# Kernel tuning notes

Hardware: AMD Instinct MI355X
Metric: run time of the kernel (lower is better)

## Reference

```python
import jax, jax.numpy as jnp
import numpy as np

N = 100000      # nodes
E = 1600000     # nnz of precomputed A^K (avg degree 16)
D = 64          # in_feats
C = 64          # n_classes
LN_EPS = 1e-5


def setup_inputs() -> dict:
    key = jax.random.key(0)
    ks = jax.random.split(key, 8)
    feat = jax.random.normal(ks[0], (N, D), dtype=jnp.float32)
    feat_ori = jax.random.normal(ks[1], (N, D), dtype=jnp.float32)
    row = jax.random.randint(ks[2], (E,), 0, N)
    col = jax.random.randint(ks[3], (E,), 0, N)
    adj_vals = jax.random.uniform(ks[4], (E,), dtype=jnp.float32)
    # Linear params (xavier_uniform weight, zero bias)
    limit = float(np.sqrt(6.0 / (D + C)))
    W = jax.random.uniform(ks[5], (C, D), dtype=jnp.float32, minval=-limit, maxval=limit)
    b = jnp.zeros((C,), dtype=jnp.float32)
    # LayerNorm params
    gamma = jnp.ones((C,), dtype=jnp.float32)
    beta = jnp.zeros((C,), dtype=jnp.float32)
    return {"feat": feat, "feat_ori": feat_ori, "row": row, "col": col,
            "adj_vals": adj_vals, "W": W, "b": b, "gamma": gamma, "beta": beta}


def reference(feat, feat_ori, row, col, adj_vals, W, b, gamma, beta):
    # NOTE: in the source, h = (1-alpha)*feat + alpha*feat_ori is dead code
    # (immediately overwritten by the SpMM of raw feat), so it is omitted.
    # SpMM: h[i] = sum_{e: row[e]=i} adj_vals[e] * feat[col[e]]   -> [N, D]
    msgs = adj_vals[:, None] * feat[col]            # [E, D] gather + scale
    h = jax.ops.segment_sum(msgs, row, num_segments=N)  # [N, D] scatter-add
    # Dense Linear: [N, D] @ [D, C] + [C]
    h = jnp.einsum('nd,cd->nc', h, W) + b
    # LayerNorm over last dim
    mu = jnp.mean(h, axis=-1, keepdims=True)
    var = jnp.mean(jnp.square(h - mu), axis=-1, keepdims=True)
    h = (h - mu) * jax.lax.rsqrt(var + LN_EPS) * gamma + beta
    return h
```

## Files before the change

### kernel.cpp

```cpp
#include <hip/hip_runtime.h>


typedef unsigned int u32;
typedef unsigned short u16;
typedef unsigned long long u64;
#define RFL(x) __builtin_amdgcn_readfirstlane(x)

#define NBLKC 64
#define MAXBK 2048
#define CAP 2048

__device__ __forceinline__ float bf2f(u16 v) {
    return __uint_as_float((u32)v << 16);
}
__device__ __forceinline__ u16 f2bf(float f) {
    u32 b = __float_as_uint(f);
    return (u16)((b + 0x7FFFu + ((b >> 16) & 1u)) >> 16);
}

__global__ __launch_bounds__(256) void k_bhist(const int* __restrict__ row,
                                               u32* __restrict__ hist2d,
                                               int E, int NBK, int CH) {
    __shared__ u32 cnt[MAXBK];
    int tid = threadIdx.x;
    for (int i = tid; i < NBK; i += 256) cnt[i] = 0;
    __syncthreads();
    int e0 = blockIdx.x * CH;
    int e1 = e0 + CH; if (e1 > E) e1 = E;
    int ev = e1 & ~3;
    for (int i = e0 + tid * 4; i < ev; i += 1024) {
        int4 r = *reinterpret_cast<const int4*>(&row[i]);
        atomicAdd(&cnt[(u32)r.x >> 6], 1u);
        atomicAdd(&cnt[(u32)r.y >> 6], 1u);
        atomicAdd(&cnt[(u32)r.z >> 6], 1u);
        atomicAdd(&cnt[(u32)r.w >> 6], 1u);
    }
    { int i = ev + tid; if (i < e1) atomicAdd(&cnt[(u32)row[i] >> 6], 1u); }
    __syncthreads();
    u32* dst = hist2d + (size_t)blockIdx.x * NBK;
    for (int i = tid; i < NBK; i += 256) dst[i] = cnt[i];
}

__device__ __forceinline__ u32 blk_scan256(u32 v, u32* wsum, u32& total) {
    int lane = threadIdx.x & 63, wid = threadIdx.x >> 6;
    u32 incl = v;
#pragma unroll
    for (int o = 1; o < 64; o <<= 1) {
        u32 u = __shfl_up(incl, o);
        if (lane >= o) incl += u;
    }
    if (lane == 63) wsum[wid] = incl;
    __syncthreads();
    u32 woff = 0;
    for (int w = 0; w < wid; ++w) woff += wsum[w];
    total = wsum[0] + wsum[1] + wsum[2] + wsum[3];
    __syncthreads();
    return woff + incl - v;
}

__global__ __launch_bounds__(256) void k_bscan(u32* __restrict__ hist2d,
                                               u32* __restrict__ btot,
                                               int NBLK, int NBK) {
    __shared__ u32 wsum[4];
    int bkt = blockIdx.x;
    u32 carry = 0;
    for (int r = 0; r < NBLK; r += 256) {
        int blk = r + threadIdx.x;
        u32 v = (blk < NBLK) ? hist2d[(size_t)blk * NBK + bkt] : 0;
        u32 tot;
        u32 ex = blk_scan256(v, wsum, tot);
        if (blk < NBLK) hist2d[(size_t)blk * NBK + bkt] = ex + carry;
        carry += tot;
    }
    if (threadIdx.x == 0) btot[bkt] = carry;
}

__global__ __launch_bounds__(256) void k_scanb2(const u32* __restrict__ btot,
                                                u32* __restrict__ bbase,
                                                int NBK, int E) {
    __shared__ u32 wsum[4];
    u32 carry = 0;
    for (int r = 0; r < NBK; r += 256) {
        int i = r + threadIdx.x;
        u32 v = (i < NBK) ? btot[i] : 0;
        u32 tot;
        u32 ex = blk_scan256(v, wsum, tot);
        if (i < NBK) bbase[i] = ex + carry;
        carry += tot;
    }
    if (threadIdx.x == 0) bbase[NBK] = (u32)E;
}

__global__ __launch_bounds__(256) void k_scatgemm(
    const int* __restrict__ row, const int* __restrict__ col,
    const float* __restrict__ vals, const u32* __restrict__ hist2d,
    const u32* __restrict__ bbase, u64* __restrict__ epair1,
    const float* __restrict__ feat, const float* __restrict__ W,
    u16* __restrict__ G, int E, int N, int NBK, int NBLK, int CH)
{
    __shared__ __align__(16) u32 smem[4096];
    int tid = threadIdx.x;
    if ((int)blockIdx.x < NBLK) {
        u32* lbase = smem;
        u32* lcnt  = smem + NBK;
        int blk = blockIdx.x;
        const u32* hrow = hist2d + (size_t)blk * NBK;
        for (int i = tid; i < NBK; i += 256) {
            lbase[i] = bbase[i] + hrow[i];
            lcnt[i] = 0;
        }
        __syncthreads();
        int e0 = blk * CH;
        int e1 = e0 + CH; if (e1 > E) e1 = E;
        int ev = e1 & ~3;
        for (int i = e0 + tid * 4; i < ev; i += 1024) {
            int4 r = *reinterpret_cast<const int4*>(&row[i]);
            int4 c = *reinterpret_cast<const int4*>(&col[i]);
            float4 v = *reinterpret_cast<const float4*>(&vals[i]);
            u32 k0 = (u32)r.x >> 6, k1 = (u32)r.y >> 6;
            u32 k2 = (u32)r.z >> 6, k3 = (u32)r.w >> 6;
            u32 q0 = atomicAdd(&lcnt[k0], 1u);
            u32 q1 = atomicAdd(&lcnt[k1], 1u);
            u32 q2 = atomicAdd(&lcnt[k2], 1u);
            u32 q3 = atomicAdd(&lcnt[k3], 1u);
            epair1[lbase[k0] + q0] = (u64)((u32)c.x | (((u32)r.x & 63u) << 26))
                                   | ((u64)__float_as_uint(v.x) << 32);
            epair1[lbase[k1] + q1] = (u64)((u32)c.y | (((u32)r.y & 63u) << 26))
                                   | ((u64)__float_as_uint(v.y) << 32);
            epair1[lbase[k2] + q2] = (u64)((u32)c.z | (((u32)r.z & 63u) << 26))
                                   | ((u64)__float_as_uint(v.z) << 32);
            epair1[lbase[k3] + q3] = (u64)((u32)c.w | (((u32)r.w & 63u) << 26))
                                   | ((u64)__float_as_uint(v.w) << 32);
        }
        {
            int i = ev + tid;
            if (i < e1) {
                u32 r = (u32)row[i];
                u32 k = r >> 6;
                u32 q = atomicAdd(&lcnt[k], 1u);
                epair1[lbase[k] + q] = (u64)((u32)col[i] | ((r & 63u) << 26))
                                     | ((u64)__float_as_uint(vals[i]) << 32);
            }
        }
    } else {
        float* fs = (float*)smem;
        int lane = tid & 63, wid = tid >> 6;
        int n0 = ((int)blockIdx.x - NBLK) * 64;
        int valid = N - n0; if (valid > 64) valid = 64;
        int elems = valid * 64;
        for (int idx = tid * 4; idx < elems; idx += 1024)
            *reinterpret_cast<float4*>(&fs[idx]) =
                *reinterpret_cast<const float4*>(&feat[(size_t)n0 * 64 + idx]);
        float wr[64];
#pragma unroll
        for (int d4 = 0; d4 < 16; ++d4) {
            float4 w4 = *reinterpret_cast<const float4*>(&W[lane * 64 + d4 * 4]);
            wr[d4 * 4 + 0] = w4.x; wr[d4 * 4 + 1] = w4.y;
            wr[d4 * 4 + 2] = w4.z; wr[d4 * 4 + 3] = w4.w;
        }
        __syncthreads();
        for (int j = 0; j < 16; ++j) {
            int r = wid * 16 + j;
            if (r >= valid) break;
            float o = 0.f;
#pragma unroll
            for (int d4 = 0; d4 < 16; ++d4) {
                float4 h4 = *reinterpret_cast<const float4*>(&fs[r * 64 + d4 * 4]);
                o = fmaf(h4.x, wr[d4 * 4 + 0], o);
                o = fmaf(h4.y, wr[d4 * 4 + 1], o);
                o = fmaf(h4.z, wr[d4 * 4 + 2], o);
                o = fmaf(h4.w, wr[d4 * 4 + 3], o);
            }
            G[(size_t)(n0 + r) * 64 + lane] = f2bf(o);
        }
    }
}

__global__ __launch_bounds__(256) void k_node2(
    const u16* __restrict__ G, const u64* __restrict__ epair1,
    const u32* __restrict__ bbase, const float* __restrict__ bias,
    const float* __restrict__ gamma, const float* __restrict__ beta,
    float* __restrict__ out, int N)
{
    __shared__ u64 sp[CAP];
    __shared__ u32 cnt[64], base[64], cnt2[64];
    int tid = threadIdx.x, lane = tid & 63, wid = tid >> 6;
    int bkt = blockIdx.x;
    if (tid < 64) { cnt[tid] = 0; cnt2[tid] = 0; }
    __syncthreads();
    int s = RFL((int)bbase[bkt]);
    int t = RFL((int)bbase[bkt + 1]);
    int m = t - s;
    bool fits = (m <= CAP);

    const u32* meta1 = (const u32*)epair1;
    for (int i = s + tid; i < t; i += 256)
        atomicAdd(&cnt[meta1[2 * (size_t)i] >> 26], 1u);
    __syncthreads();
    if (tid < 64) {
        u32 v = cnt[tid];
        u32 incl = v;
#pragma unroll
        for (int o = 1; o < 64; o <<= 1) {
            u32 u = __shfl_up(incl, o);
            if (tid >= o) incl += u;
        }
        base[tid] = incl - v;
    }
    __syncthreads();
    if (fits) {
        for (int i = s + tid; i < t; i += 256) {
            u64 p = epair1[i];
            u32 mm = (u32)p;
            u32 r = mm >> 26;
            u32 rank = atomicAdd(&cnt2[r], 1u);
            sp[base[r] + rank] = (p & 0xFFFFFFFF00000000ull) | (u64)(mm & 0x03FFFFFFu);
        }
    }
    __syncthreads();

    int rbase = bkt << 6;
    for (int j = 0; j < 16; ++j) {
        int r = wid * 16 + j;
        int n = rbase + r;
        if (n >= N) break;
        float acc0 = 0.f, acc1 = 0.f;
        if (fits) {
            int e0 = base[r], e1 = base[r] + cnt[r];
            int i = e0;
            for (; i + 8 <= e1; i += 8) {
                u64 p0 = sp[i],     p1 = sp[i + 1];
                u64 p2 = sp[i + 2], p3 = sp[i + 3];
                u64 p4 = sp[i + 4], p5 = sp[i + 5];
                u64 p6 = sp[i + 6], p7 = sp[i + 7];
                u32 c0 = RFL((u32)p0), b0 = RFL((u32)(p0 >> 32));
                u32 c1 = RFL((u32)p1), b1 = RFL((u32)(p1 >> 32));
                u32 c2 = RFL((u32)p2), b2 = RFL((u32)(p2 >> 32));
                u32 c3 = RFL((u32)p3), b3 = RFL((u32)(p3 >> 32));
                u32 c4 = RFL((u32)p4), b4 = RFL((u32)(p4 >> 32));
                u32 c5 = RFL((u32)p5), b5 = RFL((u32)(p5 >> 32));
                u32 c6 = RFL((u32)p6), b6 = RFL((u32)(p6 >> 32));
                u32 c7 = RFL((u32)p7), b7 = RFL((u32)(p7 >> 32));
                float g0 = bf2f(G[((size_t)c0 << 6) | lane]);
                float g1 = bf2f(G[((size_t)c1 << 6) | lane]);
                float g2 = bf2f(G[((size_t)c2 << 6) | lane]);
                float g3 = bf2f(G[((size_t)c3 << 6) | lane]);
                float g4 = bf2f(G[((size_t)c4 << 6) | lane]);
                float g5 = bf2f(G[((size_t)c5 << 6) | lane]);
                float g6 = bf2f(G[((size_t)c6 << 6) | lane]);
                float g7 = bf2f(G[((size_t)c7 << 6) | lane]);
                acc0 = fmaf(__uint_as_float(b0), g0, acc0);
                acc1 = fmaf(__uint_as_float(b1), g1, acc1);
                acc0 = fmaf(__uint_as_float(b2), g2, acc0);
                acc1 = fmaf(__uint_as_float(b3), g3, acc1);
                acc0 = fmaf(__uint_as_float(b4), g4, acc0);
                acc1 = fmaf(__uint_as_float(b5), g5, acc1);
                acc0 = fmaf(__uint_as_float(b6), g6, acc0);
                acc1 = fmaf(__uint_as_float(b7), g7, acc1);
            }
            for (; i < e1; ++i) {
                u64 p = sp[i];
                u32 c = RFL((u32)p), b = RFL((u32)(p >> 32));
                acc0 = fmaf(__uint_as_float(b), bf2f(G[((size_t)c << 6) | lane]), acc0);
            }
        } else {
            for (int i = s; i < t; ++i) {
                u64 p = epair1[i];
                u32 mm = RFL((u32)p);
                if ((int)(mm >> 26) == r) {
                    u32 b = RFL((u32)(p >> 32));
                    acc0 = fmaf(__uint_as_float(b),
                                bf2f(G[((size_t)(mm & 0x03FFFFFFu) << 6) | lane]), acc0);
                }
            }
        }
        float o = acc0 + acc1 + bias[lane];

        float ssum = o;
#pragma unroll
        for (int off = 32; off; off >>= 1) ssum += __shfl_xor(ssum, off);
        float mu = ssum * 0.015625f;
        float dv = o - mu;
        float vs = dv * dv;
#pragma unroll
        for (int off = 32; off; off >>= 1) vs += __shfl_xor(vs, off);
        float inv = rsqrtf(vs * 0.015625f + 1e-5f);
        out[((size_t)n << 6) + lane] = dv * inv * gamma[lane] + beta[lane];
    }
}

extern "C" void kernel_launch(void* const* d_in, const int* in_sizes, int n_in,
                              void* d_out, int out_size, void* d_ws, size_t ws_size,
                              hipStream_t stream) {
    const float* feat  = (const float*)d_in[0];
    const int*   row   = (const int*)d_in[2];
    const int*   col   = (const int*)d_in[3];
    const float* vals  = (const float*)d_in[4];
    const float* W     = (const float*)d_in[5];
    const float* bias  = (const float*)d_in[6];
    const float* gamma = (const float*)d_in[7];
    const float* beta  = (const float*)d_in[8];
    float* out = (float*)d_out;

    const int D = 64;
    int N = in_sizes[0] / D;
    int E = in_sizes[2];

    int NBK  = (N + 63) / 64;
    int NBLK = NBLKC;
    int CH   = (((E + NBLK - 1) / NBLK) + 3) & ~3;
    int NG   = (N + 63) / 64;

    char* ws = (char*)d_ws;
    u16*   G      = (u16*)ws;
    size_t off1   = (((size_t)N * 128) + 255) & ~(size_t)255;
    u64*   epair1 = (u64*)(ws + off1);
    size_t off2   = off1 + (((size_t)E * 8 + 255) & ~(size_t)255);
    u32*   hist2d = (u32*)(ws + off2);
    size_t off3   = off2 + (((size_t)NBLK * NBK * 4 + 255) & ~(size_t)255);
    u32*   btot   = (u32*)(ws + off3);
    u32*   bbase  = btot + NBK;

    k_bhist   <<<NBLK, 256, 0, stream>>>(row, hist2d, E, NBK, CH);
    k_bscan   <<<NBK, 256, 0, stream>>>(hist2d, btot, NBLK, NBK);
    k_scanb2  <<<1, 256, 0, stream>>>(btot, bbase, NBK, E);
    k_scatgemm<<<NBLK + NG, 256, 0, stream>>>(row, col, vals, hist2d, bbase,
                                              epair1, feat, W, G,
                                              E, N, NBK, NBLK, CH);
    k_node2   <<<NBK, 256, 0, stream>>>(G, epair1, bbase, bias, gamma, beta,
                                        out, N);
}
```

Measured before the change: 130.2 us.

## Split each node bucket across two blocks and break GEMM FMA dependency chain

The final aggregation kernel now launches two blocks per 64-node bucket. Each block handles 32 rows, stages only its half of the edges in a smaller shared buffer, and does 8 rows per wave instead of 16. Both blocks still histogram the whole bucket, so that work is duplicated, but parallelism doubles and shared memory per block shrinks, which should help occupancy. Separately, the dense GEMM dot product now uses four independent accumulators to shorten the serial FMA dependency chain, at the cost of slightly different rounding.

```diff
diff --git a/kernel.cpp b/kernel.cpp
--- a/kernel.cpp
+++ b/kernel.cpp
@@ -8,7 +8,7 @@
 
 #define NBLKC 64
 #define MAXBK 2048
-#define CAP 2048
+#define CAP 1280
 
 __device__ __forceinline__ float bf2f(u16 v) {
     return __uint_as_float((u32)v << 16);
@@ -162,16 +162,16 @@
         for (int j = 0; j < 16; ++j) {
             int r = wid * 16 + j;
             if (r >= valid) break;
-            float o = 0.f;
+            float oa[4] = {0.f, 0.f, 0.f, 0.f};
 #pragma unroll
             for (int d4 = 0; d4 < 16; ++d4) {
                 float4 h4 = *reinterpret_cast<const float4*>(&fs[r * 64 + d4 * 4]);
-                o = fmaf(h4.x, wr[d4 * 4 + 0], o);
-                o = fmaf(h4.y, wr[d4 * 4 + 1], o);
-                o = fmaf(h4.z, wr[d4 * 4 + 2], o);
-                o = fmaf(h4.w, wr[d4 * 4 + 3], o);
-            }
-            G[(size_t)(n0 + r) * 64 + lane] = f2bf(o);
+                oa[d4 & 3] = fmaf(h4.x, wr[d4 * 4 + 0],
+                            fmaf(h4.y, wr[d4 * 4 + 1],
+                            fmaf(h4.z, wr[d4 * 4 + 2],
+                            fmaf(h4.w, wr[d4 * 4 + 3], oa[d4 & 3]))));
+            }
+            G[(size_t)(n0 + r) * 64 + lane] = f2bf((oa[0] + oa[1]) + (oa[2] + oa[3]));
         }
     }
 }
@@ -183,15 +183,15 @@
     float* __restrict__ out, int N)
 {
     __shared__ u64 sp[CAP];
-    __shared__ u32 cnt[64], base[64], cnt2[64];
+    __shared__ u32 cnt[64], base[64], cnt2[32];
     int tid = threadIdx.x, lane = tid & 63, wid = tid >> 6;
-    int bkt = blockIdx.x;
-    if (tid < 64) { cnt[tid] = 0; cnt2[tid] = 0; }
+    int bkt  = blockIdx.x >> 1;
+    int half = blockIdx.x & 1;
+    if (tid < 64) cnt[tid] = 0;
+    if (tid < 32) cnt2[tid] = 0;
     __syncthreads();
     int s = RFL((int)bbase[bkt]);
     int t = RFL((int)bbase[bkt + 1]);
-    int m = t - s;
-    bool fits = (m <= CAP);
 
     const u32* meta1 = (const u32*)epair1;
     for (int i = s + tid; i < t; i += 256)
@@ -208,25 +208,35 @@
         base[tid] = incl - v;
     }
     __syncthreads();
+    int r0 = half << 5;
+    int myoff = base[r0];
+    int myend = (half ? (t - s) : base[32]);
+    int myedges = myend - myoff;
+    bool fits = (myedges <= CAP);
+
     if (fits) {
         for (int i = s + tid; i < t; i += 256) {
             u64 p = epair1[i];
             u32 mm = (u32)p;
             u32 r = mm >> 26;
-            u32 rank = atomicAdd(&cnt2[r], 1u);
-            sp[base[r] + rank] = (p & 0xFFFFFFFF00000000ull) | (u64)(mm & 0x03FFFFFFu);
-        }
-    }
-    __syncthreads();
-
-    int rbase = bkt << 6;
-    for (int j = 0; j < 16; ++j) {
-        int r = wid * 16 + j;
-        int n = rbase + r;
+            if ((int)(r >> 5) == half) {
+                u32 rank = atomicAdd(&cnt2[r & 31u], 1u);
+                sp[base[r] - myoff + rank] =
+                    (p & 0xFFFFFFFF00000000ull) | (u64)(mm & 0x03FFFFFFu);
+            }
+        }
+    }
+    __syncthreads();
+
+    int rbase = (bkt << 6) + r0;
+    for (int j = 0; j < 8; ++j) {
+        int rr = (wid << 3) + j;
+        int r = r0 + rr;
+        int n = rbase + rr;
         if (n >= N) break;
         float acc0 = 0.f, acc1 = 0.f;
         if (fits) {
-            int e0 = base[r], e1 = base[r] + cnt[r];
+            int e0 = base[r] - myoff, e1 = e0 + cnt[r];
             int i = e0;
             for (; i + 8 <= e1; i += 8) {
                 u64 p0 = sp[i],     p1 = sp[i + 1];
@@ -327,6 +337,6 @@
     k_scatgemm<<<NBLK + NG, 256, 0, stream>>>(row, col, vals, hist2d, bbase,
                                               epair1, feat, W, G,
                                               E, N, NBK, NBLK, CH);
-    k_node2   <<<NBK, 256, 0, stream>>>(G, epair1, bbase, bias, gamma, beta,
-                                        out, N);
-}
+    k_node2   <<<NBK * 2, 256, 0, stream>>>(G, epair1, bbase, bias, gamma,
+                                            beta, out, N);
+}
```

Result: slower. 134.2 us (+3.1%).
